# Kernel tuning notes

Hardware: AMD Instinct MI355X
Metric: run time of the kernel (lower is better)

The kernel has to match this reference:

```python
import jax, jax.numpy as jnp
import numpy as np

EPS = 1e-8
TEMP = 0.2
HOPS = 2


def _inv_sqrt_deg(deg):
    # deg^-0.5 with inf -> 0 (isolated nodes)
    return jnp.where(deg > 0, jax.lax.rsqrt(jnp.maximum(deg, 1.0)) * jnp.where(deg > 0, 1.0, 0.0), 0.0)


def gcn_conv(h, u, v, W, b, n):
    # PyG GCNConv: add self-loops, symmetric normalization, aggr='add'
    h = h @ W  # [N, out]
    loops = jnp.arange(n, dtype=u.dtype)
    uu = jnp.concatenate([u, loops])
    vv = jnp.concatenate([v, loops])
    deg = jax.ops.segment_sum(jnp.ones_like(vv, dtype=h.dtype), vv, num_segments=n)
    dis = _inv_sqrt_deg(deg)
    norm = dis[uu] * dis[vv]  # [E+N]
    out = jax.ops.segment_sum(norm[:, None] * h[uu], vv, num_segments=n)
    return out + b


def compute_message_passing(u, v, x, n, hop=HOPS):
    # to_undirected: concat edges with their flips; remove self-loops via mask
    uu = jnp.concatenate([u, v])
    vv = jnp.concatenate([v, u])
    mask = (uu != vv).astype(x.dtype)
    deg = jax.ops.segment_sum(mask, vv, num_segments=n)
    dis = _inv_sqrt_deg(deg)
    norm = dis[uu] * dis[vv] * mask  # zero out self-loop edges
    for _ in range(hop):
        x = jax.ops.segment_sum(norm[:, None] * x[uu], vv, num_segments=n)
    return x


def _cos_sim(a, b):
    na = jnp.maximum(jnp.sqrt(jnp.sum(a * a, axis=-1)), EPS)
    nb = jnp.maximum(jnp.sqrt(jnp.sum(b * b, axis=-1)), EPS)
    return jnp.sum(a * b, axis=-1) / (na * nb)


def setup_inputs() -> dict:
    key = jax.random.key(0)
    ks = jax.random.split(key, 10)
    N, E, B = 100_000, 800_000, 100_000
    Din, H, Dout = 256, 256, 64
    x = jax.random.normal(ks[0], (N, Din), dtype=jnp.float32)
    src = jax.random.randint(ks[1], (E,), 0, N, dtype=jnp.int32)
    off = jax.random.randint(ks[2], (E,), 1, N, dtype=jnp.int32)
    dst = (src + off) % N  # guaranteed no self-loops
    edge_index = jnp.stack([src, dst])  # [2, E]
    batch = jax.random.randint(ks[3], (B, 3), 0, N, dtype=jnp.int32)
    s1, s2, sp = 1.0 / np.sqrt(Din), 1.0 / np.sqrt(H), 1.0 / np.sqrt(H)
    W1 = jax.random.normal(ks[4], (Din, H), dtype=jnp.float32) * s1
    b1 = jnp.zeros((H,), jnp.float32)
    W2 = jax.random.normal(ks[5], (H, H), dtype=jnp.float32) * s2
    b2 = jnp.zeros((H,), jnp.float32)
    Wp = jax.random.normal(ks[6], (H, Dout), dtype=jnp.float32) * sp
    bp = jnp.zeros((Dout,), jnp.float32)
    return {"x": x, "edge_index": edge_index, "batch": batch,
            "W1": W1, "b1": b1, "W2": W2, "b2": b2, "Wp": Wp, "bp": bp}


def reference(x, edge_index, batch, W1, b1, W2, b2, Wp, bp):
    n = x.shape[0]
    u, v = edge_index[0], edge_index[1]
    # gnn_encoder: 2-layer GCN
    h = jax.nn.relu(gcn_conv(x, u, v, W1, b1, n))
    h = gcn_conv(h, u, v, W2, b2, n)
    # graph_pred_linear
    node_emb = h @ Wp + bp  # [N, Dout]
    # 2-hop degree-normalized propagation on the undirected graph
    all_emb = compute_message_passing(u, v, node_emb, n)
    anc = all_emb[batch[:, 0]]
    pos = all_emb[batch[:, 1]]
    neg = all_emb[batch[:, 2]]
    xs = jnp.exp(_cos_sim(anc, pos) / TEMP)
    ys = jnp.exp(_cos_sim(anc, neg) / TEMP)
    loss = -jnp.log(xs / (xs + ys))
    return loss.mean()
```

## Files before the change

kernel.cpp:

```cpp
#include <hip/hip_runtime.h>
#include <hip/hip_bf16.h>

#define DIN 256
#define HID 256
#define DOUT 64
#define NPART 8
#define BPP 256
#define CCAP 32

typedef short short8 __attribute__((ext_vector_type(8)));
typedef float f32x4 __attribute__((ext_vector_type(4)));
typedef float f32x2 __attribute__((ext_vector_type(2)));

__device__ __forceinline__ float b2f(ushort u) {
    unsigned int x = ((unsigned int)u) << 16;
    return __builtin_bit_cast(float, x);
}
__device__ __forceinline__ ushort f2bf(float f) {
    unsigned int u = __builtin_bit_cast(unsigned int, f);
    unsigned int r = (u + 0x7FFFu + ((u >> 16) & 1u)) >> 16;
    return (ushort)r;
}
__device__ __forceinline__ unsigned int cvt_pk(float lo, float hi) {
    unsigned int r;
    asm("v_cvt_pk_bf16_f32 %0, %1, %2" : "=v"(r) : "v"(lo), "v"(hi));
    return r;
}
__device__ __forceinline__ unsigned char f2fp8(float v) {
    int p = __builtin_amdgcn_cvt_pk_fp8_f32(v, v, 0, false);
    return (unsigned char)(p & 0xff);
}
__device__ __forceinline__ ushort f2fp8x2(float lo, float hi) {
    int p = __builtin_amdgcn_cvt_pk_fp8_f32(lo, hi, 0, false);
    return (ushort)(p & 0xffff);
}
__device__ __forceinline__ void gload16(const void* g, void* l) {
    __builtin_amdgcn_global_load_lds(
        (const __attribute__((address_space(1))) unsigned int*)g,
        (__attribute__((address_space(3))) unsigned int*)l, 16, 0, 0);
}
__device__ __forceinline__ int swz8(int lane, int r) {
    return (((lane >> 1) ^ (r & 7)) << 4) + (lane & 1) * 8;
}

__global__ __launch_bounds__(256) void fill_kernel(const int* __restrict__ u,
                                                   const int* __restrict__ v,
                                                   int* __restrict__ cnt_in,
                                                   int* __restrict__ cnt_out,
                                                   int* __restrict__ col_in,
                                                   int* __restrict__ col_out,
                                                   int E, unsigned pdiv) {
    const int part = blockIdx.x & (NPART - 1);
    const int step = BPP * 256;
    int e = (blockIdx.x >> 3) * 256 + threadIdx.x;

#define PROC(aa, bb)                                                  \
    do {                                                              \
        if ((unsigned)(bb) / pdiv == (unsigned)part) {                \
            int s_ = atomicAdd(&cnt_in[bb], 1);                       \
            if (s_ < CCAP) col_in[(bb) * CCAP + s_] = (aa);           \
        }                                                             \
        if ((unsigned)(aa) / pdiv == (unsigned)part) {                \
            int s_ = atomicAdd(&cnt_out[aa], 1);                      \
            if (s_ < CCAP) col_out[(aa) * CCAP + s_] = (bb);          \
        }                                                             \
    } while (0)

    for (; e + 3 * step < E; e += 4 * step) {
        int a0 = u[e],            b0 = v[e];
        int a1 = u[e + step],     b1 = v[e + step];
        int a2 = u[e + 2 * step], b2 = v[e + 2 * step];
        int a3 = u[e + 3 * step], b3 = v[e + 3 * step];
        PROC(a0, b0);
        PROC(a1, b1);
        PROC(a2, b2);
        PROC(a3, b3);
    }
    for (; e < E; e += step) {
        int a = u[e], b = v[e];
        PROC(a, b);
    }
#undef PROC
}

__global__ __launch_bounds__(256) void prep_small_kernel(
    const float* __restrict__ W1, const float* __restrict__ W2,
    const float* __restrict__ Wp,
    const int* __restrict__ cnt_in, const int* __restrict__ cnt_out,
    char* __restrict__ w1t, char* __restrict__ w2t, char* __restrict__ wpt,
    float* __restrict__ dis_g, float* __restrict__ dis_m,
    int N, int ndisb) {
    if (blockIdx.x < (unsigned)ndisb) {
        int i = blockIdx.x * 256 + threadIdx.x;
        if (i < N) {
            int ci = cnt_in[i];
            dis_g[i] = rsqrtf((float)ci + 1.0f);
            int dm = ci + cnt_out[i];
            dis_m[i] = (dm > 0) ? rsqrtf((float)dm) : 0.0f;
        }
        return;
    }
    int row = blockIdx.x - ndisb;
    const float* W; char* Wt; int NOUT;
    if (row < 256)      { W = W1; Wt = w1t; NOUT = 256; }
    else if (row < 512) { W = W2; Wt = w2t; NOUT = 256; row -= 256; }
    else                { W = Wp; Wt = wpt; NOUT = 64;  row -= 512; }
    int k = threadIdx.x;
    *(ushort*)(Wt + (size_t)row * 512 + (((k >> 3) ^ (row & 7)) << 4) + (k & 7) * 2)
        = f2bf(W[k * NOUT + row]);
}

template <int NT, int TN, int OUTMODE, bool ADD_BIAS, bool A_F32>
__global__ __launch_bounds__(512) void mfma_gemm_v7(
    const void* __restrict__ A, const char* __restrict__ Bt,
    const float* __restrict__ bias, const float* __restrict__ rowscale,
    void* __restrict__ C, int M) {
    constexpr int BM = 64;
    constexpr int TILES = NT / TN;
    constexpr int FM = (TN == 128) ? 2 : 1;
    constexpr int FN = 2;
    __shared__ __align__(16) char As[BM * 512];
    __shared__ __align__(16) char Bs[TN * 512];
    const int tid = threadIdx.x;
    const int w = tid >> 6;
    const int lane = tid & 63;
    const int row0 = blockIdx.x * BM;
    const int wrow = (TN == 128) ? ((w >> 2) * 32) : ((w >> 1) * 16);
    const int wcol = (TN == 128) ? ((w & 3) * 32) : ((w & 1) * 32);
    const int g = lane >> 4;
    const int r15 = lane & 15;
    const int wb = w * 1024;

    if (A_F32) {
        const float* Af = (const float*)A;
        int r = tid >> 3;
        int c8 = tid & 7;
        int gr = row0 + r;
        gr = (gr < M) ? gr : (M - 1);
        const float* src = Af + (size_t)gr * 256 + c8 * 8;
#pragma unroll
        for (int k = 0; k < 4; ++k) {
            float4 f0 = *(const float4*)(src + k * 64);
            float4 f1 = *(const float4*)(src + k * 64 + 4);
            uint4 pv;
            pv.x = cvt_pk(f0.x, f0.y);
            pv.y = cvt_pk(f0.z, f0.w);
            pv.z = cvt_pk(f1.x, f1.y);
            pv.w = cvt_pk(f1.z, f1.w);
            int chunk = (c8 + 8 * k) ^ (r & 7);
            *(uint4*)(As + r * 512 + (chunk << 4)) = pv;
        }
    } else {
        const char* gA = (const char*)A + (size_t)row0 * 512;
#pragma unroll
        for (int i = 0; i < BM / 16; ++i)
            gload16(gA + i * 8192 + wb + lane * 16, As + i * 8192 + wb);
    }
    {
        const char* gB = Bt;
#pragma unroll
        for (int i = 0; i < TN / 16; ++i)
            gload16(gB + i * 8192 + wb + lane * 16, Bs + i * 8192 + wb);
    }

#pragma unroll
    for (int t = 0; t < TILES; ++t) {
        __syncthreads();

        f32x4 acc[FM][FN];
#pragma unroll
        for (int m = 0; m < FM; ++m)
#pragma unroll
            for (int n = 0; n < FN; ++n) acc[m][n] = {0.f, 0.f, 0.f, 0.f};

#pragma unroll
        for (int ks = 0; ks < 8; ++ks) {
            short8 a[FM], b[FN];
#pragma unroll
            for (int m = 0; m < FM; ++m) {
                int rl = wrow + m * 16 + r15;
                a[m] = *(const short8*)(As + rl * 512 + (((ks * 4 + g) ^ (rl & 7)) << 4));
            }
#pragma unroll
            for (int n = 0; n < FN; ++n) {
                int cl = wcol + n * 16 + r15;
                b[n] = *(const short8*)(Bs + cl * 512 + (((ks * 4 + g) ^ (cl & 7)) << 4));
            }
#pragma unroll
            for (int m = 0; m < FM; ++m)
#pragma unroll
                for (int n = 0; n < FN; ++n)
                    acc[m][n] = __builtin_amdgcn_mfma_f32_16x16x32_bf16(a[m], b[n], acc[m][n], 0, 0, 0);
        }

        __syncthreads();
        if (t + 1 < TILES) {
            const char* gB = Bt + (size_t)((t + 1) * TN) * 512;
#pragma unroll
            for (int i = 0; i < TN / 16; ++i)
                gload16(gB + i * 8192 + wb + lane * 16, Bs + i * 8192 + wb);
        }

#pragma unroll
        for (int m = 0; m < FM; ++m) {
            int rbase = row0 + wrow + m * 16 + g * 4;
#pragma unroll
            for (int j = 0; j < 4; ++j) {
                int grow = rbase + j;
                if (grow >= M) continue;
                float rs = rowscale[grow];
#pragma unroll
                for (int n = 0; n < FN; ++n) {
                    int gcol = t * TN + wcol + n * 16 + r15;
                    float vv = acc[m][n][j];
                    if (ADD_BIAS) vv += bias[gcol];
                    vv *= rs;
                    if (OUTMODE == 2)
                        ((unsigned char*)C)[(size_t)grow * 256 + gcol] = f2fp8(vv);
                    else
                        ((unsigned char*)C)[(size_t)grow * 64 + gcol] = f2fp8(vv);
                }
            }
        }
    }
}

template <bool RELU>
__global__ __launch_bounds__(256) void conv_gather_fp8(const unsigned char* __restrict__ h,
                                                       const float* __restrict__ dis,
                                                       const float* __restrict__ bias,
                                                       const int* __restrict__ cnt_in,
                                                       const int* __restrict__ col_in,
                                                       char* __restrict__ out,
                                                       int N) {
    int wid = (blockIdx.x * blockDim.x + threadIdx.x) >> 6;
    int lane = threadIdx.x & 63;
    if (wid >= N) return;
    float a0, a1, a2, a3;
    {
        unsigned q = *(const unsigned*)(h + (size_t)wid * 256 + lane * 4);
        f32x2 lo = __builtin_amdgcn_cvt_pk_f32_fp8((int)q, false);
        f32x2 hi = __builtin_amdgcn_cvt_pk_f32_fp8((int)q, true);
        a0 = lo.x; a1 = lo.y; a2 = hi.x; a3 = hi.y;
    }
    const int* list = col_in + (size_t)wid * CCAP;
    int cnt = cnt_in[wid];
    cnt = (cnt < CCAP) ? cnt : CCAP;
    int e = 0;
    for (; e + 7 < cnt; e += 8) {
        unsigned q0 = *(const unsigned*)(h + (size_t)list[e + 0] * 256 + lane * 4);
        unsigned q1 = *(const unsigned*)(h + (size_t)list[e + 1] * 256 + lane * 4);
        unsigned q2 = *(const unsigned*)(h + (size_t)list[e + 2] * 256 + lane * 4);
        unsigned q3 = *(const unsigned*)(h + (size_t)list[e + 3] * 256 + lane * 4);
        unsigned q4 = *(const unsigned*)(h + (size_t)list[e + 4] * 256 + lane * 4);
        unsigned q5 = *(const unsigned*)(h + (size_t)list[e + 5] * 256 + lane * 4);
        unsigned q6 = *(const unsigned*)(h + (size_t)list[e + 6] * 256 + lane * 4);
        unsigned q7 = *(const unsigned*)(h + (size_t)list[e + 7] * 256 + lane * 4);
#pragma unroll
        for (unsigned q : {q0, q1, q2, q3, q4, q5, q6, q7}) {
            f32x2 lo = __builtin_amdgcn_cvt_pk_f32_fp8((int)q, false);
            f32x2 hi = __builtin_amdgcn_cvt_pk_f32_fp8((int)q, true);
            a0 += lo.x; a1 += lo.y; a2 += hi.x; a3 += hi.y;
        }
    }
    for (; e < cnt; ++e) {
        unsigned q = *(const unsigned*)(h + (size_t)list[e] * 256 + lane * 4);
        f32x2 lo = __builtin_amdgcn_cvt_pk_f32_fp8((int)q, false);
        f32x2 hi = __builtin_amdgcn_cvt_pk_f32_fp8((int)q, true);
        a0 += lo.x; a1 += lo.y; a2 += hi.x; a3 += hi.y;
    }
    float di = dis[wid];
    float4 bv = ((const float4*)bias)[lane];
    float o0 = di * a0 + bv.x;
    float o1 = di * a1 + bv.y;
    float o2 = di * a2 + bv.z;
    float o3 = di * a3 + bv.w;
    if (RELU) {
        o0 = fmaxf(o0, 0.f); o1 = fmaxf(o1, 0.f);
        o2 = fmaxf(o2, 0.f); o3 = fmaxf(o3, 0.f);
    }
    uint2 ov;
    ov.x = cvt_pk(o0, o1);
    ov.y = cvt_pk(o2, o3);
    *(uint2*)(out + (size_t)wid * 512 + swz8(lane, wid)) = ov;
}

template <int POW>
__global__ __launch_bounds__(256) void mp_gather_fp8(const unsigned char* __restrict__ in,
                                                     const float* __restrict__ dis,
                                                     const int* __restrict__ cnt_in,
                                                     const int* __restrict__ cnt_out,
                                                     const int* __restrict__ col_in,
                                                     const int* __restrict__ col_out,
                                                     unsigned char* __restrict__ out,
                                                     int N) {
    int wid = (blockIdx.x * blockDim.x + threadIdx.x) >> 6;
    int lane = threadIdx.x & 63;
    if (wid >= N) return;
    const int half = lane >> 5;
    const int l2 = lane & 31;
    const int* list;
    int cnt;
    if (half == 0) {
        list = col_in + (size_t)wid * CCAP;
        cnt = cnt_in[wid];
    } else {
        list = col_out + (size_t)wid * CCAP;
        cnt = cnt_out[wid];
    }
    cnt = (cnt < CCAP) ? cnt : CCAP;
    float a0 = 0.f, a1 = 0.f;
    int e = 0;
    for (; e + 3 < cnt; e += 4) {
        int s0 = list[e], s1 = list[e + 1], s2 = list[e + 2], s3 = list[e + 3];
        ushort q0 = *(const ushort*)(in + (size_t)s0 * 64 + l2 * 2);
        ushort q1 = *(const ushort*)(in + (size_t)s1 * 64 + l2 * 2);
        ushort q2 = *(const ushort*)(in + (size_t)s2 * 64 + l2 * 2);
        ushort q3 = *(const ushort*)(in + (size_t)s3 * 64 + l2 * 2);
        f32x2 f0 = __builtin_amdgcn_cvt_pk_f32_fp8((int)q0, false);
        f32x2 f1 = __builtin_amdgcn_cvt_pk_f32_fp8((int)q1, false);
        f32x2 f2 = __builtin_amdgcn_cvt_pk_f32_fp8((int)q2, false);
        f32x2 f3 = __builtin_amdgcn_cvt_pk_f32_fp8((int)q3, false);
        a0 += f0.x + f1.x + f2.x + f3.x;
        a1 += f0.y + f1.y + f2.y + f3.y;
    }
    for (; e < cnt; ++e) {
        int s = list[e];
        ushort q = *(const ushort*)(in + (size_t)s * 64 + l2 * 2);
        f32x2 f = __builtin_amdgcn_cvt_pk_f32_fp8((int)q, false);
        a0 += f.x;
        a1 += f.y;
    }
    a0 += __shfl_xor(a0, 32);
    a1 += __shfl_xor(a1, 32);
    if (half == 0) {
        float d = dis[wid];
        float sc = (POW == 2) ? d * d : d;
        *(ushort*)(out + (size_t)wid * 64 + l2 * 2) = f2fp8x2(sc * a0, sc * a1);
    }
}

__global__ __launch_bounds__(256) void loss_kernel(const unsigned char* __restrict__ emb,
                                                   const int* __restrict__ batch,
                                                   float* __restrict__ out,
                                                   int B, float invB) {
    const int nhw = gridDim.x * 8;
    const int hwid = blockIdx.x * 8 + (threadIdx.x >> 5);
    const int l2 = threadIdx.x & 31;
    float lsum = 0.0f;
    for (int r = hwid; r < B; r += nhw) {
        int a = batch[r * 3 + 0];
        int p = batch[r * 3 + 1];
        int ng = batch[r * 3 + 2];
        ushort qa = *(const ushort*)(emb + (size_t)a * 64 + l2 * 2);
        ushort qp = *(const ushort*)(emb + (size_t)p * 64 + l2 * 2);
        ushort qn = *(const ushort*)(emb + (size_t)ng * 64 + l2 * 2);
        f32x2 fa = __builtin_amdgcn_cvt_pk_f32_fp8((int)qa, false);
        f32x2 fp = __builtin_amdgcn_cvt_pk_f32_fp8((int)qp, false);
        f32x2 fn = __builtin_amdgcn_cvt_pk_f32_fp8((int)qn, false);
        float aa = fa.x * fa.x + fa.y * fa.y;
        float pp = fp.x * fp.x + fp.y * fp.y;
        float nn = fn.x * fn.x + fn.y * fn.y;
        float ap = fa.x * fp.x + fa.y * fp.y;
        float an = fa.x * fn.x + fa.y * fn.y;
#pragma unroll
        for (int off = 16; off > 0; off >>= 1) {
            aa += __shfl_xor(aa, off);
            pp += __shfl_xor(pp, off);
            nn += __shfl_xor(nn, off);
            ap += __shfl_xor(ap, off);
            an += __shfl_xor(an, off);
        }
        if (l2 == 0) {
            float na = fmaxf(sqrtf(aa), 1e-8f);
            float npp = fmaxf(sqrtf(pp), 1e-8f);
            float nnn = fmaxf(sqrtf(nn), 1e-8f);
            float cx = ap / (na * npp);
            float cy = an / (na * nnn);
            lsum += log1pf(expf((cy - cx) * 5.0f));
        }
    }
    __shared__ float part[8];
    if (l2 == 0) part[threadIdx.x >> 5] = lsum;
    __syncthreads();
    if (threadIdx.x == 0) {
        float s = 0.f;
#pragma unroll
        for (int i = 0; i < 8; ++i) s += part[i];
        atomicAdd(out, s * invB);
    }
}

extern "C" void kernel_launch(void* const* d_in, const int* in_sizes, int n_in,
                              void* d_out, int out_size, void* d_ws, size_t ws_size,
                              hipStream_t stream) {
    const float* x   = (const float*)d_in[0];
    const int* ei    = (const int*)d_in[1];
    const int* batch = (const int*)d_in[2];
    const float* W1  = (const float*)d_in[3];
    const float* b1  = (const float*)d_in[4];
    const float* W2  = (const float*)d_in[5];
    const float* b2  = (const float*)d_in[6];
    const float* Wp  = (const float*)d_in[7];
    const float* bp  = (const float*)d_in[8];
    const int N = in_sizes[0] / DIN;
    const int E = in_sizes[1] / 2;
    const int B = in_sizes[2] / 3;
    const int* u = ei;
    const int* v = ei + E;
    const unsigned pdiv = (unsigned)((N + NPART - 1) / NPART);

    char* aggb    = (char*)d_ws;
    unsigned char* hb = (unsigned char*)(aggb + (size_t)N * 512);
    unsigned char* embA = hb + (size_t)N * 256;
    unsigned char* embB = embA + (size_t)N * 64;
    char* w1t     = (char*)(embB + (size_t)N * 64);
    char* w2t     = w1t + 256 * 512;
    char* wpt     = w2t + 256 * 512;
    float* dis_g  = (float*)(wpt + 64 * 512);
    float* dis_m  = dis_g + N;
    int* cnt_in   = (int*)(dis_m + N);
    int* cnt_out  = cnt_in + N;
    int* col_in   = cnt_out + N;
    int* col_out  = col_in + (size_t)N * CCAP;

    const int nwb = (N + 3) / 4;
    const int ndisb = (N + 255) / 256;
    const int gm = (N + 63) / 64;

    hipMemsetAsync(cnt_in, 0, 2 * (size_t)N * sizeof(int), stream);
    fill_kernel<<<NPART * BPP, 256, 0, stream>>>(u, v, cnt_in, cnt_out,
                                                 col_in, col_out, E, pdiv);

    prep_small_kernel<<<ndisb + 576, 256, 0, stream>>>(
        W1, W2, Wp, cnt_in, cnt_out, w1t, w2t, wpt, dis_g, dis_m, N, ndisb);

    mfma_gemm_v7<256, 64, 2, false, true><<<gm, 512, 0, stream>>>(
        x, w1t, nullptr, dis_g, hb, N);
    conv_gather_fp8<true><<<nwb, 256, 0, stream>>>(hb, dis_g, b1, cnt_in, col_in, aggb, N);

    mfma_gemm_v7<256, 128, 2, false, false><<<gm, 512, 0, stream>>>(
        aggb, w2t, nullptr, dis_g, hb, N);
    conv_gather_fp8<false><<<nwb, 256, 0, stream>>>(hb, dis_g, b2, cnt_in, col_in, aggb, N);

    mfma_gemm_v7<64, 64, 3, true, false><<<gm, 512, 0, stream>>>(
        aggb, wpt, bp, dis_m, embA, N);

    mp_gather_fp8<2><<<nwb, 256, 0, stream>>>(embA, dis_m, cnt_in, cnt_out,
                                              col_in, col_out, embB, N);
    mp_gather_fp8<1><<<nwb, 256, 0, stream>>>(embB, dis_m, cnt_in, cnt_out,
                                              col_in, col_out, embA, N);

    hipMemsetAsync(d_out, 0, sizeof(float), stream);
    loss_kernel<<<1024, 256, 0, stream>>>(embA, batch, (float*)d_out, B, 1.0f / (float)B);
}
```

Measured before the change: 457.4 us.

## Co-schedule CSR fill with first GEMM in one fused launch

Merges the edge-bucketing fill kernel and the first x@W1 GEMM into a single launch whose blocks are interleaved, so the atomic-bound fill overlaps with the compute-bound GEMM. Because dis_g is no longer known when the first GEMM runs, the GEMM drops its row scaling, and the first conv gather instead multiplies each neighbour's fp8 row by that neighbour's dis value. The weight cast and the degree computation become separate small kernels. The price is an extra per-neighbour dis load in the gather, one more launch, and fp8 quantisation of unscaled values.

Measured after the change: 433.5 us. 1.06x faster.

```diff
diff --git a/kernel.cpp b/kernel.cpp
--- a/kernel.cpp
+++ b/kernel.cpp
@@ -5,7 +5,7 @@
 #define HID 256
 #define DOUT 64
 #define NPART 8
-#define BPP 256
+#define FPB 128
 #define CCAP 32
 
 typedef short short8 __attribute__((ext_vector_type(8)));
@@ -43,16 +43,17 @@
     return (((lane >> 1) ^ (r & 7)) << 4) + (lane & 1) * 8;
 }
 
-__global__ __launch_bounds__(256) void fill_kernel(const int* __restrict__ u,
-                                                   const int* __restrict__ v,
-                                                   int* __restrict__ cnt_in,
-                                                   int* __restrict__ cnt_out,
-                                                   int* __restrict__ col_in,
-                                                   int* __restrict__ col_out,
-                                                   int E, unsigned pdiv) {
-    const int part = blockIdx.x & (NPART - 1);
-    const int step = BPP * 256;
-    int e = (blockIdx.x >> 3) * 256 + threadIdx.x;
+__device__ __forceinline__ void fill_body(int fid,
+                                          const int* __restrict__ u,
+                                          const int* __restrict__ v,
+                                          int* __restrict__ cnt_in,
+                                          int* __restrict__ cnt_out,
+                                          int* __restrict__ col_in,
+                                          int* __restrict__ col_out,
+                                          int E, unsigned pdiv) {
+    const int part = fid & (NPART - 1);
+    const int step = FPB * 512;
+    int e = (fid >> 3) * 512 + threadIdx.x;
 
 #define PROC(aa, bb)                                                  \
     do {                                                              \
@@ -83,35 +84,9 @@
 #undef PROC
 }
 
-__global__ __launch_bounds__(256) void prep_small_kernel(
-    const float* __restrict__ W1, const float* __restrict__ W2,
-    const float* __restrict__ Wp,
-    const int* __restrict__ cnt_in, const int* __restrict__ cnt_out,
-    char* __restrict__ w1t, char* __restrict__ w2t, char* __restrict__ wpt,
-    float* __restrict__ dis_g, float* __restrict__ dis_m,
-    int N, int ndisb) {
-    if (blockIdx.x < (unsigned)ndisb) {
-        int i = blockIdx.x * 256 + threadIdx.x;
-        if (i < N) {
-            int ci = cnt_in[i];
-            dis_g[i] = rsqrtf((float)ci + 1.0f);
-            int dm = ci + cnt_out[i];
-            dis_m[i] = (dm > 0) ? rsqrtf((float)dm) : 0.0f;
-        }
-        return;
-    }
-    int row = blockIdx.x - ndisb;
-    const float* W; char* Wt; int NOUT;
-    if (row < 256)      { W = W1; Wt = w1t; NOUT = 256; }
-    else if (row < 512) { W = W2; Wt = w2t; NOUT = 256; row -= 256; }
-    else                { W = Wp; Wt = wpt; NOUT = 64;  row -= 512; }
-    int k = threadIdx.x;
-    *(ushort*)(Wt + (size_t)row * 512 + (((k >> 3) ^ (row & 7)) << 4) + (k & 7) * 2)
-        = f2bf(W[k * NOUT + row]);
-}
-
-template <int NT, int TN, int OUTMODE, bool ADD_BIAS, bool A_F32>
-__global__ __launch_bounds__(512) void mfma_gemm_v7(
+template <int NT, int TN, int OUTMODE, bool ADD_BIAS, bool A_F32, bool SCALE>
+__device__ __forceinline__ void gemm_body(
+    int bidx, char* As, char* Bs,
     const void* __restrict__ A, const char* __restrict__ Bt,
     const float* __restrict__ bias, const float* __restrict__ rowscale,
     void* __restrict__ C, int M) {
@@ -119,12 +94,10 @@
     constexpr int TILES = NT / TN;
     constexpr int FM = (TN == 128) ? 2 : 1;
     constexpr int FN = 2;
-    __shared__ __align__(16) char As[BM * 512];
-    __shared__ __align__(16) char Bs[TN * 512];
     const int tid = threadIdx.x;
     const int w = tid >> 6;
     const int lane = tid & 63;
-    const int row0 = blockIdx.x * BM;
+    const int row0 = bidx * BM;
     const int wrow = (TN == 128) ? ((w >> 2) * 32) : ((w >> 1) * 16);
     const int wcol = (TN == 128) ? ((w & 3) * 32) : ((w & 1) * 32);
     const int g = lane >> 4;
@@ -208,13 +181,13 @@
             for (int j = 0; j < 4; ++j) {
                 int grow = rbase + j;
                 if (grow >= M) continue;
-                float rs = rowscale[grow];
+                float rs = SCALE ? rowscale[grow] : 1.0f;
 #pragma unroll
                 for (int n = 0; n < FN; ++n) {
                     int gcol = t * TN + wcol + n * 16 + r15;
                     float vv = acc[m][n][j];
                     if (ADD_BIAS) vv += bias[gcol];
-                    vv *= rs;
+                    if (SCALE) vv *= rs;
                     if (OUTMODE == 2)
                         ((unsigned char*)C)[(size_t)grow * 256 + gcol] = f2fp8(vv);
                     else
@@ -225,7 +198,80 @@
     }
 }
 
-template <bool RELU>
+__global__ __launch_bounds__(512) void fill_gemm1_kernel(
+    const int* __restrict__ u, const int* __restrict__ v,
+    int* __restrict__ cnt_in, int* __restrict__ cnt_out,
+    int* __restrict__ col_in, int* __restrict__ col_out,
+    int E, unsigned pdiv,
+    const float* __restrict__ x, const char* __restrict__ w1t,
+    unsigned char* __restrict__ hb, int M,
+    int gG, int gF, int nG, int nF) {
+    __shared__ __align__(16) char As[64 * 512];
+    __shared__ __align__(16) char Bs[64 * 512];
+    const int G = blockIdx.x >> 3;
+    const int sub = blockIdx.x & 7;
+    const int gmin = (gG < gF) ? gG : gF;
+    bool isG;
+    int idx;
+    if (G < 2 * gmin) {
+        isG = ((G & 1) == 0);
+        idx = (G >> 1) * 8 + sub;
+    } else if (gG > gF) {
+        isG = true;
+        idx = (G - gmin) * 8 + sub;
+    } else {
+        isG = false;
+        idx = (G - gmin) * 8 + sub;
+    }
+    if (isG) {
+        if (idx < nG)
+            gemm_body<256, 64, 2, false, true, false>(idx, As, Bs, x, w1t,
+                                                      nullptr, nullptr, hb, M);
+    } else {
+        if (idx < nF)
+            fill_body(idx, u, v, cnt_in, cnt_out, col_in, col_out, E, pdiv);
+    }
+}
+
+template <int NT, int TN, int OUTMODE, bool ADD_BIAS, bool A_F32>
+__global__ __launch_bounds__(512) void mfma_gemm_v7(
+    const void* __restrict__ A, const char* __restrict__ Bt,
+    const float* __restrict__ bias, const float* __restrict__ rowscale,
+    void* __restrict__ C, int M) {
+    __shared__ __align__(16) char As[64 * 512];
+    __shared__ __align__(16) char Bs[TN * 512];
+    gemm_body<NT, TN, OUTMODE, ADD_BIAS, A_F32, true>(
+        blockIdx.x, As, Bs, A, Bt, bias, rowscale, C, M);
+}
+
+__global__ __launch_bounds__(256) void wcast_kernel(
+    const float* __restrict__ W1, const float* __restrict__ W2,
+    const float* __restrict__ Wp,
+    char* __restrict__ w1t, char* __restrict__ w2t, char* __restrict__ wpt) {
+    int row = blockIdx.x;
+    const float* W; char* Wt; int NOUT;
+    if (row < 256)      { W = W1; Wt = w1t; NOUT = 256; }
+    else if (row < 512) { W = W2; Wt = w2t; NOUT = 256; row -= 256; }
+    else                { W = Wp; Wt = wpt; NOUT = 64;  row -= 512; }
+    int k = threadIdx.x;
+    *(ushort*)(Wt + (size_t)row * 512 + (((k >> 3) ^ (row & 7)) << 4) + (k & 7) * 2)
+        = f2bf(W[k * NOUT + row]);
+}
+
+__global__ __launch_bounds__(256) void dis_kernel(const int* __restrict__ cnt_in,
+                                                  const int* __restrict__ cnt_out,
+                                                  float* __restrict__ dis_g,
+                                                  float* __restrict__ dis_m,
+                                                  int N) {
+    int i = blockIdx.x * blockDim.x + threadIdx.x;
+    if (i >= N) return;
+    int ci = cnt_in[i];
+    dis_g[i] = rsqrtf((float)ci + 1.0f);
+    int dm = ci + cnt_out[i];
+    dis_m[i] = (dm > 0) ? rsqrtf((float)dm) : 0.0f;
+}
+
+template <bool RELU, bool NEIGH_DIS>
 __global__ __launch_bounds__(256) void conv_gather_fp8(const unsigned char* __restrict__ h,
                                                        const float* __restrict__ dis,
                                                        const float* __restrict__ bias,
@@ -236,40 +282,45 @@
     int wid = (blockIdx.x * blockDim.x + threadIdx.x) >> 6;
     int lane = threadIdx.x & 63;
     if (wid >= N) return;
+    float di = dis[wid];
     float a0, a1, a2, a3;
     {
         unsigned q = *(const unsigned*)(h + (size_t)wid * 256 + lane * 4);
         f32x2 lo = __builtin_amdgcn_cvt_pk_f32_fp8((int)q, false);
         f32x2 hi = __builtin_amdgcn_cvt_pk_f32_fp8((int)q, true);
-        a0 = lo.x; a1 = lo.y; a2 = hi.x; a3 = hi.y;
+        float ws = NEIGH_DIS ? di : 1.0f;
+        a0 = ws * lo.x; a1 = ws * lo.y; a2 = ws * hi.x; a3 = ws * hi.y;
     }
     const int* list = col_in + (size_t)wid * CCAP;
     int cnt = cnt_in[wid];
     cnt = (cnt < CCAP) ? cnt : CCAP;
     int e = 0;
     for (; e + 7 < cnt; e += 8) {
-        unsigned q0 = *(const unsigned*)(h + (size_t)list[e + 0] * 256 + lane * 4);
-        unsigned q1 = *(const unsigned*)(h + (size_t)list[e + 1] * 256 + lane * 4);
-        unsigned q2 = *(const unsigned*)(h + (size_t)list[e + 2] * 256 + lane * 4);
-        unsigned q3 = *(const unsigned*)(h + (size_t)list[e + 3] * 256 + lane * 4);
-        unsigned q4 = *(const unsigned*)(h + (size_t)list[e + 4] * 256 + lane * 4);
-        unsigned q5 = *(const unsigned*)(h + (size_t)list[e + 5] * 256 + lane * 4);
-        unsigned q6 = *(const unsigned*)(h + (size_t)list[e + 6] * 256 + lane * 4);
-        unsigned q7 = *(const unsigned*)(h + (size_t)list[e + 7] * 256 + lane * 4);
-#pragma unroll
-        for (unsigned q : {q0, q1, q2, q3, q4, q5, q6, q7}) {
-            f32x2 lo = __builtin_amdgcn_cvt_pk_f32_fp8((int)q, false);
-            f32x2 hi = __builtin_amdgcn_cvt_pk_f32_fp8((int)q, true);
-            a0 += lo.x; a1 += lo.y; a2 += hi.x; a3 += hi.y;
+        int ss[8];
+        unsigned qs[8];
+#pragma unroll
+        for (int k = 0; k < 8; ++k) ss[k] = list[e + k];
+#pragma unroll
+        for (int k = 0; k < 8; ++k)
+            qs[k] = *(const unsigned*)(h + (size_t)ss[k] * 256 + lane * 4);
+#pragma unroll
+        for (int k = 0; k < 8; ++k) {
+            float wgt = NEIGH_DIS ? dis[ss[k]] : 1.0f;
+            f32x2 lo = __builtin_amdgcn_cvt_pk_f32_fp8((int)qs[k], false);
+            f32x2 hi = __builtin_amdgcn_cvt_pk_f32_fp8((int)qs[k], true);
+            a0 += wgt * lo.x; a1 += wgt * lo.y;
+            a2 += wgt * hi.x; a3 += wgt * hi.y;
         }
     }
     for (; e < cnt; ++e) {
-        unsigned q = *(const unsigned*)(h + (size_t)list[e] * 256 + lane * 4);
+        int s = list[e];
+        float wgt = NEIGH_DIS ? dis[s] : 1.0f;
+        unsigned q = *(const unsigned*)(h + (size_t)s * 256 + lane * 4);
         f32x2 lo = __builtin_amdgcn_cvt_pk_f32_fp8((int)q, false);
         f32x2 hi = __builtin_amdgcn_cvt_pk_f32_fp8((int)q, true);
-        a0 += lo.x; a1 += lo.y; a2 += hi.x; a3 += hi.y;
-    }
-    float di = dis[wid];
+        a0 += wgt * lo.x; a1 += wgt * lo.y;
+        a2 += wgt * hi.x; a3 += wgt * hi.y;
+    }
     float4 bv = ((const float4*)bias)[lane];
     float o0 = di * a0 + bv.x;
     float o1 = di * a1 + bv.y;
@@ -429,19 +480,25 @@
     const int gm = (N + 63) / 64;
 
     hipMemsetAsync(cnt_in, 0, 2 * (size_t)N * sizeof(int), stream);
-    fill_kernel<<<NPART * BPP, 256, 0, stream>>>(u, v, cnt_in, cnt_out,
-                                                 col_in, col_out, E, pdiv);
-
-    prep_small_kernel<<<ndisb + 576, 256, 0, stream>>>(
-        W1, W2, Wp, cnt_in, cnt_out, w1t, w2t, wpt, dis_g, dis_m, N, ndisb);
-
-    mfma_gemm_v7<256, 64, 2, false, true><<<gm, 512, 0, stream>>>(
-        x, w1t, nullptr, dis_g, hb, N);
-    conv_gather_fp8<true><<<nwb, 256, 0, stream>>>(hb, dis_g, b1, cnt_in, col_in, aggb, N);
+    wcast_kernel<<<576, 256, 0, stream>>>(W1, W2, Wp, w1t, w2t, wpt);
+
+    const int nG = gm;
+    const int gG = (nG + 7) / 8;
+    const int nF = NPART * FPB;
+    const int gF = nF / 8;
+    fill_gemm1_kernel<<<(gG + gF) * 8, 512, 0, stream>>>(
+        u, v, cnt_in, cnt_out, col_in, col_out, E, pdiv,
+        x, w1t, hb, N, gG, gF, nG, nF);
+
+    dis_kernel<<<ndisb, 256, 0, stream>>>(cnt_in, cnt_out, dis_g, dis_m, N);
+
+    conv_gather_fp8<true, true><<<nwb, 256, 0, stream>>>(
+        hb, dis_g, b1, cnt_in, col_in, aggb, N);
 
     mfma_gemm_v7<256, 128, 2, false, false><<<gm, 512, 0, stream>>>(
         aggb, w2t, nullptr, dis_g, hb, N);
-    conv_gather_fp8<false><<<nwb, 256, 0, stream>>>(hb, dis_g, b2, cnt_in, col_in, aggb, N);
+    conv_gather_fp8<false, false><<<nwb, 256, 0, stream>>>(
+        hb, dis_g, b2, cnt_in, col_in, aggb, N);
 
     mfma_gemm_v7<64, 64, 3, true, false><<<gm, 512, 0, stream>>>(
         aggb, wpt, bp, dis_m, embA, N);
```
